# Performance work log

Hardware: AMD Instinct MI355X
Metric: run time of the kernel (lower is better)

## Reference

```python
import jax, jax.numpy as jnp
import numpy as np

NUM_SAMPLE = 80  # hardcoded in the original forward
NUM_ACT = 6
NUM_OPP = 3


def setup_inputs() -> dict:
    key = jax.random.key(0)
    k0, k1, k2 = jax.random.split(key, 3)
    B, D = 4096, 512
    x = jax.random.normal(k0, (B, D), dtype=jnp.float32)
    # orthogonal init with gain 0.01 -> small weights; approximate scale
    W_opp = jax.random.normal(k1, (NUM_OPP, D, NUM_ACT), dtype=jnp.float32) * 0.01
    b_opp = jnp.zeros((NUM_OPP, NUM_ACT), dtype=jnp.float32)
    W = jax.random.normal(k2, (D + NUM_OPP * NUM_ACT, NUM_ACT), dtype=jnp.float32) * 0.01
    b = jnp.zeros((NUM_ACT,), dtype=jnp.float32)
    return {"x": x, "W_opp": W_opp, "b_opp": b_opp, "W": W, "b": b}


def reference(x, W_opp, b_opp, W, b):
    B, D = x.shape
    # --- opponent actors: small linear + softmax, vectorized over the 3 opponents ---
    logits = jnp.einsum('bd,kda->kba', x, W_opp) + b_opp[:, None, :]   # [3,B,6]
    dist = jax.nn.softmax(logits, axis=-1)                              # [3,B,6]
    logp = jax.nn.log_softmax(logits, axis=-1)
    # entropy.mean() per opponent, then sum/3 == mean over opponents
    entropy = (-(dist * logp).sum(-1)).mean(-1).mean()

    # --- vectorized categorical sampling: 80 samples per opponent per batch elem ---
    skey = jax.random.key(42)
    samples = jax.random.categorical(skey, logits[:, None], axis=-1,
                                     shape=(NUM_OPP, NUM_SAMPLE, B))   # [3,S,B] int

    # gather sampled-action probabilities
    probs = jnp.take_along_axis(dist[:, None], samples[..., None], axis=-1)[..., 0]  # [3,S,B]
    probs_bt = jnp.transpose(probs, (0, 2, 1))                          # [3,B,S]
    p1 = probs_bt[0] * probs_bt[1] * probs_bt[2]                        # [B,S]
    p2 = p1 / p1.sum(axis=1, keepdims=True)                             # normalized joint weights

    # actions3[b,s,k] = sampled action of opponent k, sample s, batch b
    acts = jnp.transpose(samples, (2, 1, 0))                            # [B,S,3]
    oh = jax.nn.one_hot(acts, NUM_ACT, dtype=x.dtype).reshape(B, NUM_SAMPLE, NUM_OPP * NUM_ACT)  # [B,S,18]

    xa = jnp.broadcast_to(x[:, None, :], (B, NUM_SAMPLE, D))            # replicate x per sample
    a = jnp.concatenate([xa, oh], axis=2)                               # [B,S,D+18]
    agent_probs = jax.nn.softmax(a @ W + b, axis=-1)                    # [B,S,6]

    actions_probs = jnp.einsum('bs,bsa->ba', p2, agent_probs)           # [B,6]
    return actions_probs, dist, entropy
```

## Files before the change

kernel.cpp:

```cpp
#include <hip/hip_runtime.h>
#include <stdint.h>

#define NUM_ACT 6
#define NUM_OPP 3
#define NUM_SAMPLE 80
#define BATCH 4096
#define DIM 512
#define ENT_IDX 98304

__device__ __forceinline__ uint32_t rotl32(uint32_t x, int d) {
  return (x << d) | (x >> (32 - d));
}

__device__ __forceinline__ void tf_round4(uint32_t& x0, uint32_t& x1,
                                          int r0, int r1, int r2, int r3) {
  x0 += x1; x1 = rotl32(x1, r0); x1 ^= x0;
  x0 += x1; x1 = rotl32(x1, r1); x1 ^= x0;
  x0 += x1; x1 = rotl32(x1, r2); x1 ^= x0;
  x0 += x1; x1 = rotl32(x1, r3); x1 ^= x0;
}

__device__ __forceinline__ void threefry2x32(uint32_t k0, uint32_t k1,
                                             uint32_t& x0, uint32_t& x1) {
  const uint32_t ks2 = k0 ^ k1 ^ 0x1BD11BDAu;
  x0 += k0;  x1 += k1;
  tf_round4(x0, x1, 13, 15, 26, 6);  x0 += k1;  x1 += ks2 + 1u;
  tf_round4(x0, x1, 17, 29, 16, 24); x0 += ks2; x1 += k0  + 2u;
  tf_round4(x0, x1, 13, 15, 26, 6);  x0 += k0;  x1 += k1  + 3u;
  tf_round4(x0, x1, 17, 29, 16, 24); x0 += k1;  x1 += ks2 + 4u;
  tf_round4(x0, x1, 13, 15, 26, 6);  x0 += ks2; x1 += k0  + 5u;
}

__device__ __forceinline__ float jax_uniform(uint32_t flat_idx) {
  uint32_t x0 = 0u, x1 = flat_idx;
  threefry2x32(0u, 42u, x0, x1);
  uint32_t bits = x0 ^ x1;
  return __uint_as_float((bits >> 9) | 0x3f800000u) - 1.0f;
}

__device__ __forceinline__ void dot4(float& a, float4 u, float4 v) {
  a = fmaf(u.x, v.x, a); a = fmaf(u.y, v.y, a);
  a = fmaf(u.z, v.z, a); a = fmaf(u.w, v.w, a);
}

#define O_XS   0
#define O_WT   4352
#define O_PART 17408
#define O_W2   18944
#define O_DIST 19052
#define O_XW   19196
#define O_HW   19244

__global__ __launch_bounds__(512) void k_all(
    const float* __restrict__ x, const float* __restrict__ Wopp,
    const float* __restrict__ bopp, const float* __restrict__ W,
    const float* __restrict__ bias, float* __restrict__ out) {
  __shared__ float sm[19252];
  const int t = threadIdx.x;
  const int w = t >> 6;
  const int l = t & 63;
  const int rowbase = blockIdx.x * 8;
  const int b = rowbase + w;

  for (int u = t; u < 8 * 128; u += 512) {
    int row = u >> 7, c4 = (u & 127) << 2;
    float4 v = *(const float4*)(x + (size_t)(rowbase + row) * DIM + c4);
    *(float4*)(sm + O_XS + (c4 >> 6) * 544 + row * 68 + (c4 & 63)) = v;
  }
  for (int j = t; j < 3072; j += 512) {
    int f = j << 2;
    float4 v = (f < 9216) ? *(const float4*)(Wopp + f)
                          : *(const float4*)(W + (f - 9216));
    float vv[4] = {v.x, v.y, v.z, v.w};
#pragma unroll
    for (int e = 0; e < 4; e++) {
      int ff = f + e;
      int c, d;
      if (ff < 9216) { int k = ff / 3072, r = ff % 3072; d = r / 6; c = k * 6 + r % 6; }
      else           { int r = ff - 9216; d = r / 6; c = 18 + r % 6; }
      sm[O_WT + (d >> 6) * 1632 + c * 68 + (d & 63)] = vv[e];
    }
  }
  if (t < 54) {
    float2 v = *(const float2*)(W + DIM * NUM_ACT + 2 * t);
    sm[O_W2 + 2 * t] = v.x; sm[O_W2 + 2 * t + 1] = v.y;
  }
  __syncthreads();

  {
    const int sub = t >> 6, row = (t >> 3) & 7, colg = t & 7;
    const float* xp = sm + O_XS + sub * 544 + row * 68;
    const float* wp = sm + O_WT + sub * 1632 + (colg * 3) * 68;
    float a0 = 0.f, a1 = 0.f, a2 = 0.f;
#pragma unroll 4
    for (int dd = 0; dd < 64; dd += 4) {
      float4 xv = *(const float4*)(xp + dd);
      dot4(a0, xv, *(const float4*)(wp + dd));
      dot4(a1, xv, *(const float4*)(wp + 68 + dd));
      dot4(a2, xv, *(const float4*)(wp + 136 + dd));
    }
    float* pp = sm + O_PART + sub * 192 + row * 24 + colg * 3;
    pp[0] = a0; pp[1] = a1; pp[2] = a2;
  }
  __syncthreads();

  float colsum = 0.f;
  if (l < 24) {
    float s = (l < 18) ? bopp[l] : bias[l - 18];
#pragma unroll
    for (int g = 0; g < 8; g++)
      s += sm[O_PART + g * 192 + w * 24 + l];
    colsum = s;
    if (l >= 18) sm[O_XW + w * 6 + (l - 18)] = s;
  }
  const int kk = (l < NUM_OPP) ? l : 0;
  float lg[NUM_ACT];
#pragma unroll
  for (int a = 0; a < NUM_ACT; a++)
    lg[a] = __shfl(colsum, kk * NUM_ACT + a);

  float H = 0.f;
  if (l < NUM_OPP) {
    const int k = l;
    float m = lg[0];
#pragma unroll
    for (int a = 1; a < NUM_ACT; a++) m = fmaxf(m, lg[a]);
    float e[NUM_ACT], Z = 0.f;
#pragma unroll
    for (int a = 0; a < NUM_ACT; a++) { e[a] = expf(lg[a] - m); Z += e[a]; }
    float logZ = logf(Z);
#pragma unroll
    for (int a = 0; a < NUM_ACT; a++) {
      float pa = e[a] / Z;
      sm[O_DIST + w * 18 + k * NUM_ACT + a] = pa;
      H -= pa * ((lg[a] - m) - logZ);
    }
  }
  H += __shfl_down(H, 1);
  H += __shfl_down(H, 2);
  if (l == 0) sm[O_HW + w] = H;

  __syncthreads();
  if (t == 0) {
    float hs = 0.f;
#pragma unroll
    for (int i = 0; i < 8; i++) hs += sm[O_HW + i];
    atomicAdd(out + ENT_IDX, hs * (1.0f / 12288.0f));
  }

  float d[18];
#pragma unroll
  for (int i = 0; i < 18; i++) d[i] = sm[O_DIST + w * 18 + i];

  int   act_a[3];
  float pr_a[3];
#pragma unroll
  for (int k = 0; k < NUM_OPP; k++) {
    float u = jax_uniform((uint32_t)(k * NUM_SAMPLE + l) * BATCH + (uint32_t)b);
    float c = d[k * 6 + 0], pr = d[k * 6 + 0];
    int sel = 0;
#pragma unroll
    for (int a = 1; a < NUM_ACT; a++) {
      bool take = (u >= c);
      sel += take ? 1 : 0;
      pr = take ? d[k * 6 + a] : pr;
      c += d[k * 6 + a];
    }
    act_a[k] = sel; pr_a[k] = pr;
  }
  float prb = 0.f; int actb = 0;
  if (l < 48) {
    const int k = l >> 4, s = 64 + (l & 15);
    float u = jax_uniform((uint32_t)(k * NUM_SAMPLE + s) * BATCH + (uint32_t)b);
    float c = sm[O_DIST + w * 18 + k * 6 + 0], pr = c;
    int sel = 0;
#pragma unroll
    for (int a = 1; a < NUM_ACT; a++) {
      float da = sm[O_DIST + w * 18 + k * 6 + a];
      bool take = (u >= c);
      sel += take ? 1 : 0;
      pr = take ? da : pr;
      c += da;
    }
    actb = sel; prb = pr;
  }
  const int tm = l & 15;
  float pb0 = __shfl(prb, tm), pb1 = __shfl(prb, tm + 16), pb2 = __shfl(prb, tm + 32);
  int   ab0 = __shfl(actb, tm), ab1 = __shfl(actb, tm + 16), ab2 = __shfl(actb, tm + 32);

  const bool hasb = l < (NUM_SAMPLE - 64);
  float p1a = pr_a[0] * pr_a[1] * pr_a[2];
  float p1b = 0.f;
  if (hasb) p1b = pb0 * pb1 * pb2;
  float tot = p1a + p1b;
#pragma unroll
  for (int m = 32; m > 0; m >>= 1) tot += __shfl_xor(tot, m);

  float xw[NUM_ACT];
#pragma unroll
  for (int a = 0; a < NUM_ACT; a++) xw[a] = sm[O_XW + w * 6 + a];

  float o[NUM_ACT];
#pragma unroll
  for (int a = 0; a < NUM_ACT; a++) o[a] = 0.f;
  {
    int a0 = act_a[0], a1 = act_a[1], a2 = act_a[2];
    float la[NUM_ACT];
#pragma unroll
    for (int a = 0; a < NUM_ACT; a++)
      la[a] = xw[a] + sm[O_W2 + a0 * 6 + a] + sm[O_W2 + (6 + a1) * 6 + a]
                    + sm[O_W2 + (12 + a2) * 6 + a];
    float m = la[0];
#pragma unroll
    for (int a = 1; a < NUM_ACT; a++) m = fmaxf(m, la[a]);
    float e[NUM_ACT], Z = 0.f;
#pragma unroll
    for (int a = 0; a < NUM_ACT; a++) { e[a] = expf(la[a] - m); Z += e[a]; }
    float wz = (p1a / tot) / Z;
#pragma unroll
    for (int a = 0; a < NUM_ACT; a++) o[a] = wz * e[a];
  }
  if (hasb) {
    float la[NUM_ACT];
#pragma unroll
    for (int a = 0; a < NUM_ACT; a++)
      la[a] = xw[a] + sm[O_W2 + ab0 * 6 + a] + sm[O_W2 + (6 + ab1) * 6 + a]
                    + sm[O_W2 + (12 + ab2) * 6 + a];
    float m = la[0];
#pragma unroll
    for (int a = 1; a < NUM_ACT; a++) m = fmaxf(m, la[a]);
    float e[NUM_ACT], Z = 0.f;
#pragma unroll
    for (int a = 0; a < NUM_ACT; a++) { e[a] = expf(la[a] - m); Z += e[a]; }
    float wz = (p1b / tot) / Z;
#pragma unroll
    for (int a = 0; a < NUM_ACT; a++) o[a] += wz * e[a];
  }
#pragma unroll
  for (int m = 32; m > 0; m >>= 1)
#pragma unroll
    for (int a = 0; a < NUM_ACT; a++) o[a] += __shfl_xor(o[a], m);

  if (l == 0) {
#pragma unroll
    for (int a = 0; a < NUM_ACT; a++) out[b * NUM_ACT + a] = o[a];
  }
  if (l < 18) {
    int k = l / 6, a = l - k * 6;
    out[BATCH * NUM_ACT + ((size_t)k * BATCH + b) * NUM_ACT + a] =
        sm[O_DIST + w * 18 + l];
  }
}

extern "C" void kernel_launch(void* const* d_in, const int* in_sizes, int n_in,
                              void* d_out, int out_size, void* d_ws, size_t ws_size,
                              hipStream_t stream) {
  const float* x    = (const float*)d_in[0];
  const float* Wopp = (const float*)d_in[1];
  const float* bopp = (const float*)d_in[2];
  const float* W    = (const float*)d_in[3];
  const float* bias = (const float*)d_in[4];
  float* out = (float*)d_out;

  hipMemsetAsync(out + ENT_IDX, 0, sizeof(float), stream);
  k_all<<<BATCH / 8, 512, 0, stream>>>(x, Wopp, bopp, W, bias, out);
}
```

Before: 81.64 us.

## Load x via direct global-to-LDS DMA with XOR swizzle and 2-row register blocking

Replaces the register-staged float4 copy of x into shared memory with direct global_load_lds transfers into an XOR-swizzled layout, removing padding and VGPR round-trips. The small matmul now uses only 256 threads, each computing two rows, so every weight float4 read is reused twice. This lowers LDS traffic but halves the threads active in that phase. The swizzle and the indexing of the per-wave LDS destination must agree exactly, or x is read incorrectly.

```diff
diff --git a/kernel.cpp b/kernel.cpp
--- a/kernel.cpp
+++ b/kernel.cpp
@@ -43,29 +43,37 @@
   a = fmaf(u.z, v.z, a); a = fmaf(u.w, v.w, a);
 }
 
+__device__ __forceinline__ void gload_lds16(const void* g, void* l) {
+  __builtin_amdgcn_global_load_lds(
+      (const __attribute__((address_space(1))) uint32_t*)g,
+      (__attribute__((address_space(3))) uint32_t*)l, 16, 0, 0);
+}
+
 #define O_XS   0
-#define O_WT   4352
-#define O_PART 17408
-#define O_W2   18944
-#define O_DIST 19052
-#define O_XW   19196
-#define O_HW   19244
+#define O_WT   4096
+#define O_PART 17152
+#define O_W2   18688
+#define O_DIST 18796
+#define O_XW   18940
+#define O_HW   18988
 
 __global__ __launch_bounds__(512) void k_all(
     const float* __restrict__ x, const float* __restrict__ Wopp,
     const float* __restrict__ bopp, const float* __restrict__ W,
     const float* __restrict__ bias, float* __restrict__ out) {
-  __shared__ float sm[19252];
+  __shared__ float sm[18996];
   const int t = threadIdx.x;
   const int w = t >> 6;
   const int l = t & 63;
   const int rowbase = blockIdx.x * 8;
   const int b = rowbase + w;
 
-  for (int u = t; u < 8 * 128; u += 512) {
-    int row = u >> 7, c4 = (u & 127) << 2;
-    float4 v = *(const float4*)(x + (size_t)(rowbase + row) * DIM + c4);
-    *(float4*)(sm + O_XS + (c4 >> 6) * 544 + row * 68 + (c4 & 63)) = v;
+#pragma unroll
+  for (int q = 0; q < 2; q++) {
+    const uint32_t s = (uint32_t)(w * 2 + q) * 1024u + (uint32_t)l * 16u;
+    const uint32_t e = s ^ (((s >> 11) & 7u) << 4);
+    const char* gp = (const char*)x + (size_t)(rowbase + (e >> 11)) * 2048 + (e & 2047u);
+    gload_lds16(gp, sm + O_XS + (w * 2 + q) * 256);
   }
   for (int j = t; j < 3072; j += 512) {
     int f = j << 2;
@@ -87,20 +95,31 @@
   }
   __syncthreads();
 
-  {
-    const int sub = t >> 6, row = (t >> 3) & 7, colg = t & 7;
-    const float* xp = sm + O_XS + sub * 544 + row * 68;
+  if (t < 256) {
+    const int sub = t >> 5;
+    const int p   = (t >> 3) & 3;
+    const int colg = t & 7;
+    const int r0 = p * 2;
     const float* wp = sm + O_WT + sub * 1632 + (colg * 3) * 68;
-    float a0 = 0.f, a1 = 0.f, a2 = 0.f;
+    const int xb0 = (r0    ) * 512 + sub * 64;
+    const int xb1 = (r0 + 1) * 512 + sub * 64;
+    const int xr0 = ((r0    ) & 7) << 2;
+    const int xr1 = ((r0 + 1) & 7) << 2;
+    float a00 = 0.f, a01 = 0.f, a02 = 0.f;
+    float a10 = 0.f, a11 = 0.f, a12 = 0.f;
 #pragma unroll 4
     for (int dd = 0; dd < 64; dd += 4) {
-      float4 xv = *(const float4*)(xp + dd);
-      dot4(a0, xv, *(const float4*)(wp + dd));
-      dot4(a1, xv, *(const float4*)(wp + 68 + dd));
-      dot4(a2, xv, *(const float4*)(wp + 136 + dd));
-    }
-    float* pp = sm + O_PART + sub * 192 + row * 24 + colg * 3;
-    pp[0] = a0; pp[1] = a1; pp[2] = a2;
+      float4 x0 = *(const float4*)(sm + O_XS + ((xb0 + dd) ^ xr0));
+      float4 x1 = *(const float4*)(sm + O_XS + ((xb1 + dd) ^ xr1));
+      float4 w0 = *(const float4*)(wp + dd);
+      float4 w1 = *(const float4*)(wp + 68 + dd);
+      float4 w2 = *(const float4*)(wp + 136 + dd);
+      dot4(a00, x0, w0); dot4(a01, x0, w1); dot4(a02, x0, w2);
+      dot4(a10, x1, w0); dot4(a11, x1, w1); dot4(a12, x1, w2);
+    }
+    float* pp = sm + O_PART + sub * 192 + r0 * 24 + colg * 3;
+    pp[0]  = a00; pp[1]  = a01; pp[2]  = a02;
+    pp[24] = a10; pp[25] = a11; pp[26] = a12;
   }
   __syncthreads();
 
```

Result: slower. 84.97 us (+4.1%).
